# Optimization experiments

Hardware: AMD Instinct MI355X
Metric: run time of the kernel (lower is better)

The kernel has to match this reference:

```python
import jax, jax.numpy as jnp
import numpy as np

EPS = 1e-6
GRID_ORDER_K = 4
DIST_K = 3


def _smallest_k(d, k):
    # k smallest values along last axis, ascending (torch.topk largest=False)
    return -jax.lax.top_k(-d, k)[0]


def _radius_loss(real, fake):
    qs = jnp.array([0.05, 0.1, 0.25, 0.5, 0.75, 0.9, 0.95], jnp.float32)
    fq = jnp.quantile(fake[:, :, 2], qs)
    rq = jnp.quantile(real[:, :, 2], qs)
    return jnp.mean((fq - rq) ** 2)


def _grid_density_loss(real, fake):
    qs = jnp.array([0.05, 0.25, 0.5, 0.75, 0.95], jnp.float32)
    lx = jnp.mean((jnp.quantile(fake[:, :, 0], qs) - jnp.quantile(real[:, :, 0], qs)) ** 2)
    ly = jnp.mean((jnp.quantile(fake[:, :, 1], qs) - jnp.quantile(real[:, :, 1], qs)) ** 2)
    return (lx + ly) / 2


def _knn_dists_flat(x, k):
    # x: [B,N,3]; pairwise dist on xy with +eps under sqrt as in source
    xy = x[:, :, :2]
    d = jnp.sqrt(((xy[:, :, None, :] - xy[:, None, :, :]) ** 2).sum(-1) + EPS)  # [B,N,N]
    d = _smallest_k(d, k)  # [B,N,k]
    return d.reshape(x.shape[0], -1)


def _distance_loss(real, fake):
    qs = jnp.array([0.05, 0.5, 0.95], jnp.float32)
    rq = jnp.quantile(_knn_dists_flat(real, DIST_K), qs, axis=1)  # [3,B]
    fq = jnp.quantile(_knn_dists_flat(fake, DIST_K), qs, axis=1)
    return jnp.mean((fq - rq) ** 2)


def _hexatic_order(coords, k):
    # coords: [B,N,2] -> psi: [B,N] complex
    B, N, _ = coords.shape
    diffs = coords[:, :, None, :] - coords[:, None, :, :]  # [B,N,N,2]
    dx = diffs[..., 0]
    dx = dx + EPS * (jnp.abs(dx) < EPS).astype(dx.dtype)
    angles = jnp.arctan2(diffs[..., 1], dx)
    e_iktheta = jnp.exp(1j * k * angles)  # [B,N,N] complex64
    dist = jnp.sqrt((diffs ** 2).sum(-1) + EPS)
    eye = jnp.eye(N, dtype=bool)[None]
    dist = jnp.where(eye, jnp.inf, dist)
    kth = jax.lax.stop_gradient(_smallest_k(dist, k)[..., -1])  # [B,N]
    sigma = jnp.maximum(0.1 * jnp.maximum(kth[..., None], EPS), EPS)
    arg = jnp.clip((kth[..., None] - dist) / sigma, -50.0, 50.0)
    w = jax.nn.sigmoid(arg)
    psi = (e_iktheta * w).sum(2) / jnp.maximum(w.sum(2), EPS)
    return psi


def _grid_order_loss(samples):
    psi = _hexatic_order(samples[:, :, :2], GRID_ORDER_K)
    return -jnp.mean(jnp.sqrt(psi * jnp.conj(psi))).real


def _physical_feasibility_loss(fake):
    xy = fake[:, :, :2]
    r = fake[:, :, 2]
    N = fake.shape[1]
    sq = ((xy[:, :, None, :] - xy[:, None, :, :]) ** 2).sum(-1)
    d = jnp.sqrt(jnp.where(sq <= 0, 1.0, sq))  # safe sqrt (guard grads at 0)
    d = jnp.where(sq <= 0, 0.0, d)
    tril = jnp.tril(jnp.ones((N, N), bool))[None]
    d = jnp.where(tril, d, 0.0)
    d = jnp.where(d <= 0, jnp.inf, d)
    radii_pair = jnp.abs(r)[:, None, :] + jnp.abs(r)[:, :, None]
    overlap = jax.nn.relu(radii_pair - (d + 1e-4))  # sqrt(x**2)==x for x>=0
    return overlap.sum() / (radii_pair.sum() / 2)


def _gan_loss(fake_outputs):
    t = 0.9  # ones_like - 0.1 label smoothing
    logp = jnp.maximum(jnp.log(fake_outputs), -100.0)
    log1mp = jnp.maximum(jnp.log(1.0 - fake_outputs), -100.0)
    return -jnp.mean(t * logp + (1.0 - t) * log1mp)


def setup_inputs() -> dict:
    key = jax.random.key(0)
    k1, k2, k3 = jax.random.split(key, 3)
    B, N = 4, 2048
    real_images = jax.random.normal(k1, (B, N, 3), jnp.float32)
    fake_images = jax.random.normal(k2, (B, N, 3), jnp.float32)
    fake_outputs = jax.random.uniform(k3, (B, 1), jnp.float32, 1e-3, 1.0 - 1e-3)
    return {"real_images": real_images, "fake_images": fake_images, "fake_outputs": fake_outputs}


def reference(real_images, fake_images, fake_outputs):
    loss = _radius_loss(real_images, fake_images)
    loss = loss + _physical_feasibility_loss(fake_images)
    loss = loss + _gan_loss(fake_outputs)
    loss = loss + _grid_density_loss(real_images, fake_images)
    loss = loss + _distance_loss(real_images, fake_images)
    loss = loss + _grid_order_loss(fake_images)
    return loss
```

## Files before the change

### kernel.cpp

```cpp
#include <hip/hip_runtime.h>
#include <math.h>

#define B_SZ   4
#define N_PTS  2048
#define EPSF   1e-6f

#define WS_KNN_R 0
#define WS_KNN_F 24576
#define WS_FEAS  49152
#define WS_PSIP  50176
#define WS_RSUM  51200
#define WS_Q     51204
#define QZF (WS_Q + 0)
#define QZR (WS_Q + 7)
#define QXF (WS_Q + 14)
#define QXR (WS_Q + 19)
#define QYF (WS_Q + 24)
#define QYR (WS_Q + 29)
#define QDR (WS_Q + 34)
#define QDF (WS_Q + 46)

__constant__ float c_qs7[7] = {0.05f, 0.1f, 0.25f, 0.5f, 0.75f, 0.9f, 0.95f};
__constant__ float c_qs5[5] = {0.05f, 0.25f, 0.5f, 0.75f, 0.95f};
__constant__ float c_qs3[3] = {0.05f, 0.5f, 0.95f};

#define CE(a, b) { float _lo = fminf(a, b), _hi = fmaxf(a, b); a = _lo; b = _hi; }

__device__ __forceinline__ void ins3a(float m[3], float v) {
    float h0 = fmaxf(m[0], v); m[0] = fminf(m[0], v);
    float h1 = fmaxf(m[1], h0); m[1] = fminf(m[1], h0);
    m[2] = fminf(m[2], h1);
}
__device__ __forceinline__ void ins5a(float m[5], float v) {
    float h0 = fmaxf(m[0], v); m[0] = fminf(m[0], v);
    float h1 = fmaxf(m[1], h0); m[1] = fminf(m[1], h0);
    float h2 = fmaxf(m[2], h1); m[2] = fminf(m[2], h1);
    float h3 = fmaxf(m[3], h2); m[3] = fminf(m[3], h2);
    m[4] = fminf(m[4], h3);
}

__device__ __forceinline__ unsigned int tokey(float f) {
    unsigned int u = __float_as_uint(f);
    return (u & 0x80000000u) ? ~u : (u | 0x80000000u);
}
__device__ __forceinline__ float fromkey(unsigned int k) {
    unsigned int u = (k & 0x80000000u) ? (k ^ 0x80000000u) : ~k;
    return __uint_as_float(u);
}

__global__ __launch_bounds__(256) void hs_pair_kernel(const float* __restrict__ real,
                                                      const float* __restrict__ fake,
                                                      float* __restrict__ ws) {
    __shared__ float2 sxy[N_PTS];
    __shared__ float sr[N_PTS];
    __shared__ float red[256];
    const int tid = threadIdx.x, wave = tid >> 6, lane = tid & 63;
    const int blk = blockIdx.x;

    if (blk < 1024) {
        const int b = blk >> 8, grp = blk & 255;
        const float* src = fake + (size_t)b * N_PTS * 3;
        for (int t = tid; t < N_PTS; t += 256) {
            const float* p = src + t * 3;
            sxy[t] = make_float2(p[0], p[1]);
            sr[t]  = fabsf(p[2]);
        }
        __syncthreads();
        const int p0 = grp * 8 + wave * 2;
        float px[2], py[2], pri[2], m[2][5];
#pragma unroll
        for (int t = 0; t < 2; ++t) {
            px[t] = sxy[p0 + t].x; py[t] = sxy[p0 + t].y;
            pri[t] = sr[p0 + t] - 1e-4f;
            m[t][0] = m[t][1] = m[t][2] = m[t][3] = m[t][4] = INFINITY;
        }
        float acc = 0.f;
        for (int j = lane; j < N_PTS; j += 64) {
            float2 q = sxy[j]; float br = sr[j];
#pragma unroll
            for (int t = 0; t < 2; ++t) {
                float dx = px[t] - q.x, dy = py[t] - q.y;
                float sq = fmaf(dx, dx, dy * dy);
                ins5a(m[t], sq);
                float ov = fmaxf((pri[t] + br) - sqrtf(sq), 0.f);
                acc += (sq > 0.f) ? ov : 0.f;
            }
        }
#pragma unroll
        for (int off = 1; off < 64; off <<= 1) {
#pragma unroll
            for (int t = 0; t < 2; ++t) {
                float b0 = __shfl_xor(m[t][0], off);
                float b1 = __shfl_xor(m[t][1], off);
                float b2 = __shfl_xor(m[t][2], off);
                float b3 = __shfl_xor(m[t][3], off);
                float b4 = __shfl_xor(m[t][4], off);
                float l0 = fminf(m[t][0], b4);
                float l1 = fminf(m[t][1], b3);
                float l2 = fminf(m[t][2], b2);
                float l3 = fminf(m[t][3], b1);
                float l4 = fminf(m[t][4], b0);
                CE(l0, l3); CE(l1, l4); CE(l0, l2); CE(l1, l3);
                CE(l0, l1); CE(l2, l4); CE(l1, l2); CE(l3, l4); CE(l2, l3);
                m[t][0] = l0; m[t][1] = l1; m[t][2] = l2; m[t][3] = l3; m[t][4] = l4;
            }
        }
        if (lane == 0) {
            float* kout = ws + WS_KNN_F + b * (N_PTS * 3);
#pragma unroll
            for (int t = 0; t < 2; ++t) {
                const int i = p0 + t;
                kout[i * 3 + 0] = sqrtf(m[t][0] + EPSF);
                kout[i * 3 + 1] = sqrtf(m[t][1] + EPSF);
                kout[i * 3 + 2] = sqrtf(m[t][2] + EPSF);
            }
        }
        float kth[2], invs[2];
#pragma unroll
        for (int t = 0; t < 2; ++t) {
            kth[t] = sqrtf(m[t][4] + EPSF);
            invs[t] = 1.f / fmaxf(0.1f * fmaxf(kth[t], EPSF), EPSF);
        }
        float sw[2], sre[2], sim[2];
#pragma unroll
        for (int t = 0; t < 2; ++t) { sw[t] = 0.f; sre[t] = 0.f; sim[t] = 0.f; }
        for (int j = lane; j < N_PTS; j += 64) {
            float2 q = sxy[j];
#pragma unroll
            for (int t = 0; t < 2; ++t) {
                float dx = px[t] - q.x, dy = py[t] - q.y;
                float sq = fmaf(dx, dx, dy * dy);
                float dist = sqrtf(sq + EPSF);
                dist = (j == p0 + t) ? INFINITY : dist;
                float a = dx + ((fabsf(dx) < EPSF) ? EPSF : 0.f);
                float arg = fminf(fmaxf((kth[t] - dist) * invs[t], -50.f), 50.f);
                float e = __expf(-arg);
                float w = __builtin_amdgcn_rcpf(1.f + e);
                float aa = a * a, bb = dy * dy;
                float n2 = aa + bb;
                float z2r = aa - bb;
                float t0 = a * dy; float z2i = t0 + t0;
                float inv = __builtin_amdgcn_rcpf(n2);
                float ur = z2r * inv, ui = z2i * inv;
                float e4r = fmaf(ur, ur, -(ui * ui));
                float t1 = ur * ui; float e4i = t1 + t1;
                sw[t] += w;
                sre[t] = fmaf(w, e4r, sre[t]);
                sim[t] = fmaf(w, e4i, sim[t]);
            }
        }
#pragma unroll
        for (int off = 1; off < 64; off <<= 1) {
#pragma unroll
            for (int t = 0; t < 2; ++t) {
                sw[t]  += __shfl_xor(sw[t], off);
                sre[t] += __shfl_xor(sre[t], off);
                sim[t] += __shfl_xor(sim[t], off);
            }
        }
        float mypsi = 0.f;
        if (lane == 0) {
#pragma unroll
            for (int t = 0; t < 2; ++t) {
                float den = fmaxf(sw[t], EPSF);
                float pr = sre[t] / den, pi = sim[t] / den;
                mypsi += sqrtf(fmaf(pr, pr, pi * pi));
            }
        }
        red[tid] = acc;
        __syncthreads();
        for (int s = 128; s > 0; s >>= 1) {
            if (tid < s) red[tid] += red[tid + s];
            __syncthreads();
        }
        if (tid == 0) ws[WS_FEAS + blk] = red[0];
        __syncthreads();
        red[tid] = (lane == 0) ? mypsi : 0.f;
        __syncthreads();
        for (int s = 128; s > 0; s >>= 1) {
            if (tid < s) red[tid] += red[tid + s];
            __syncthreads();
        }
        if (tid == 0) ws[WS_PSIP + blk] = red[0];
        if (grp == 0) {
            __syncthreads();
            float rs = 0.f;
            for (int t = tid; t < N_PTS; t += 256) rs += sr[t];
            red[tid] = rs;
            __syncthreads();
            for (int s = 128; s > 0; s >>= 1) {
                if (tid < s) red[tid] += red[tid + s];
                __syncthreads();
            }
            if (tid == 0) ws[WS_RSUM + b] = red[0];
        }
    } else {
        const int rb = blk - 1024;
        const int b = rb >> 7, grp = rb & 127;
        const float* src = real + (size_t)b * N_PTS * 3;
        for (int t = tid; t < N_PTS; t += 256) {
            const float* p = src + t * 3;
            sxy[t] = make_float2(p[0], p[1]);
        }
        __syncthreads();
        const int p0 = grp * 16 + wave * 4;
        float px[4], py[4], m[4][3];
#pragma unroll
        for (int t = 0; t < 4; ++t) {
            px[t] = sxy[p0 + t].x; py[t] = sxy[p0 + t].y;
            m[t][0] = m[t][1] = m[t][2] = INFINITY;
        }
        for (int j = lane; j < N_PTS; j += 64) {
            float2 q = sxy[j];
#pragma unroll
            for (int t = 0; t < 4; ++t) {
                float dx = px[t] - q.x, dy = py[t] - q.y;
                float sq = fmaf(dx, dx, dy * dy);
                ins3a(m[t], sq);
            }
        }
#pragma unroll
        for (int off = 1; off < 64; off <<= 1) {
#pragma unroll
            for (int t = 0; t < 4; ++t) {
                float b0 = __shfl_xor(m[t][0], off);
                float b1 = __shfl_xor(m[t][1], off);
                float b2 = __shfl_xor(m[t][2], off);
                float l0 = fminf(m[t][0], b2);
                float l1 = fminf(m[t][1], b1);
                float l2 = fminf(m[t][2], b0);
                CE(l0, l1); CE(l0, l2); CE(l1, l2);
                m[t][0] = l0; m[t][1] = l1; m[t][2] = l2;
            }
        }
        if (lane == 0) {
            float* kout = ws + WS_KNN_R + b * (N_PTS * 3);
#pragma unroll
            for (int t = 0; t < 4; ++t) {
                const int i = p0 + t;
                kout[i * 3 + 0] = sqrtf(m[t][0] + EPSF);
                kout[i * 3 + 1] = sqrtf(m[t][1] + EPSF);
                kout[i * 3 + 2] = sqrtf(m[t][2] + EPSF);
            }
        }
    }
}

__global__ __launch_bounds__(256) void hs_select_kernel(const float* __restrict__ real,
                                                        const float* __restrict__ fake,
                                                        float* __restrict__ ws) {
    __shared__ unsigned int hist[2048];
    __shared__ unsigned int wtot[4];
    __shared__ unsigned int s_bin, s_rank;
    __shared__ unsigned int s_part[4], s_min[4];
    const int tid = threadIdx.x, wave = tid >> 6, lane = tid & 63;
    const int jb = blockIdx.x;

    const float* src; int step, n, slot; float q;
    if (jb < 34) {
        int aid, qi;
        if (jb < 7)       { aid = 0; qi = jb; }
        else if (jb < 14) { aid = 1; qi = jb - 7; }
        else              { aid = 2 + (jb - 14) / 5; qi = (jb - 14) % 5; }
        const float* base = (aid & 1) ? real : fake;
        const int c = (aid < 2) ? 2 : ((aid < 4) ? 0 : 1);
        src = base + c; step = 3; n = 8192;
        q = (aid < 2) ? c_qs7[qi] : c_qs5[qi];
        slot = ((aid == 0) ? QZF : (aid == 1) ? QZR : (aid == 2) ? QXF
              : (aid == 3) ? QXR : (aid == 4) ? QYF : QYR) + qi;
    } else {
        const int a = jb - 34;
        const int side = a / 12;
        const int b = (a % 12) / 3, qi = a % 3;
        src = ws + (side ? WS_KNN_F : WS_KNN_R) + b * (N_PTS * 3);
        step = 1; n = N_PTS * 3;
        q = c_qs3[qi];
        slot = (side ? QDF : QDR) + b * 3 + qi;
    }

    unsigned int r[32];
#pragma unroll
    for (int u = 0; u < 32; ++u) {
        int e = u * 256 + tid;
        r[u] = (e < n) ? tokey(src[(size_t)e * step]) : 0xFFFFFFFFu;
    }

    const float pos = q * (float)(n - 1);
    const int k = (int)pos;
    const float frac = pos - (float)k;

    unsigned int prefix = 0;
    unsigned int kk = (unsigned int)k;
#pragma unroll
    for (int pass = 0; pass < 3; ++pass) {
        const int shift = (pass == 0) ? 21 : (pass == 1) ? 10 : 0;
        for (int i = tid; i < 2048; i += 256) hist[i] = 0u;
        __syncthreads();
#pragma unroll
        for (int u = 0; u < 32; ++u) {
            unsigned int key = r[u];
            bool act = (pass == 0) ? true
                     : (pass == 1) ? ((key >> 21) == (prefix >> 21))
                                   : ((key >> 10) == (prefix >> 10));
            if (act) atomicAdd(&hist[(key >> shift) & 2047u], 1u);
        }
        __syncthreads();
        unsigned int c[8], psum = 0;
        const int base = tid * 8;
#pragma unroll
        for (int i = 0; i < 8; ++i) { c[i] = hist[base + i]; psum += c[i]; }
        unsigned int v = psum;
#pragma unroll
        for (int off = 1; off < 64; off <<= 1) {
            unsigned int nb = (unsigned int)__shfl_up((int)v, off);
            if (lane >= off) v += nb;
        }
        if (lane == 63) wtot[wave] = v;
        __syncthreads();
        unsigned int woff = 0;
        for (int w2 = 0; w2 < wave; ++w2) woff += wtot[w2];
        unsigned int incl = v + woff;
        unsigned int excl = incl - psum;
        if (excl <= kk && kk < incl) {
            unsigned int cum = excl;
#pragma unroll
            for (int i = 0; i < 8; ++i) {
                if (kk < cum + c[i]) { s_bin = (unsigned int)(base + i); s_rank = kk - cum; break; }
                cum += c[i];
            }
        }
        __syncthreads();
        prefix |= s_bin << shift;
        kk = s_rank;
        __syncthreads();
    }
    const unsigned int vk = prefix;

    unsigned int cle = 0, mg = 0xFFFFFFFFu;
#pragma unroll
    for (int u = 0; u < 32; ++u) {
        cle += (r[u] <= vk) ? 1u : 0u;
        if (r[u] > vk && r[u] < mg) mg = r[u];
    }
#pragma unroll
    for (int off = 1; off < 64; off <<= 1) {
        cle += (unsigned int)__shfl_xor((int)cle, off);
        unsigned int om = (unsigned int)__shfl_xor((int)mg, off);
        mg = (om < mg) ? om : mg;
    }
    if (lane == 0) { s_part[wave] = cle; s_min[wave] = mg; }
    __syncthreads();
    if (tid == 0) {
        unsigned int tot = s_part[0] + s_part[1] + s_part[2] + s_part[3];
        unsigned int mga = s_min[0];
        if (s_min[1] < mga) mga = s_min[1];
        if (s_min[2] < mga) mga = s_min[2];
        if (s_min[3] < mga) mga = s_min[3];
        unsigned int vhi = (tot >= (unsigned int)(k + 2)) ? vk : mga;
        float flo = fromkey(vk), fhi = fromkey(vhi);
        ws[slot] = flo + frac * (fhi - flo);
    }
}

__global__ __launch_bounds__(256) void hs_final_kernel(const float* __restrict__ fouts,
                                                       const float* __restrict__ ws,
                                                       float* __restrict__ out) {
    __shared__ float red[256];
    __shared__ float s_feas;
    const int tid = threadIdx.x;
    float fs = 0.f, ps = 0.f;
    for (int t = tid; t < 1024; t += 256) {
        fs += ws[WS_FEAS + t];
        ps += ws[WS_PSIP + t];
    }
    red[tid] = fs;
    __syncthreads();
    for (int s = 128; s > 0; s >>= 1) {
        if (tid < s) red[tid] += red[tid + s];
        __syncthreads();
    }
    if (tid == 0) s_feas = red[0];
    __syncthreads();
    red[tid] = ps;
    __syncthreads();
    for (int s = 128; s > 0; s >>= 1) {
        if (tid < s) red[tid] += red[tid + s];
        __syncthreads();
    }
    if (tid == 0) {
        float psi_sum = red[0];
        float rsum = ws[WS_RSUM + 0] + ws[WS_RSUM + 1] + ws[WS_RSUM + 2] + ws[WS_RSUM + 3];
        float loss = 0.f;
        float sacc = 0.f;
        for (int q = 0; q < 7; ++q) { float d = ws[QZF + q] - ws[QZR + q]; sacc += d * d; }
        loss += sacc / 7.f;
        loss += (0.5f * s_feas) / ((float)N_PTS * rsum);
        float g = 0.f;
        for (int b = 0; b < B_SZ; ++b) {
            float p = fouts[b];
            g += 0.9f * fmaxf(logf(p), -100.f) + 0.1f * fmaxf(logf(1.f - p), -100.f);
        }
        loss += -g / (float)B_SZ;
        float sx = 0.f, sy = 0.f;
        for (int q = 0; q < 5; ++q) {
            float dx = ws[QXF + q] - ws[QXR + q]; sx += dx * dx;
            float dy = ws[QYF + q] - ws[QYR + q]; sy += dy * dy;
        }
        loss += 0.5f * (sx / 5.f + sy / 5.f);
        float sd = 0.f;
        for (int t = 0; t < 12; ++t) { float d = ws[QDF + t] - ws[QDR + t]; sd += d * d; }
        loss += sd / 12.f;
        loss += -psi_sum / (float)(B_SZ * N_PTS);
        out[0] = loss;
    }
}

extern "C" void kernel_launch(void* const* d_in, const int* in_sizes, int n_in,
                              void* d_out, int out_size, void* d_ws, size_t ws_size,
                              hipStream_t stream) {
    (void)in_sizes; (void)n_in; (void)out_size; (void)ws_size;
    const float* real  = (const float*)d_in[0];
    const float* fake  = (const float*)d_in[1];
    const float* fouts = (const float*)d_in[2];
    float* out = (float*)d_out;
    float* ws  = (float*)d_ws;

    hipLaunchKernelGGL(hs_pair_kernel,   dim3(1536), dim3(256), 0, stream, real, fake, ws);
    hipLaunchKernelGGL(hs_select_kernel, dim3(58),   dim3(256), 0, stream, real, fake, ws);
    hipLaunchKernelGGL(hs_final_kernel,  dim3(1),    dim3(256), 0, stream, fouts, ws, out);
}
```

Measured before the change: 121.6 us.

## Rewrite quantile select as single-wave 8-bit radix select with LDS keys

Reworks the quantile selection kernel to use one 64-lane wave per block, storing keys in shared memory and running a four-pass 8-bit radix select with replicated histograms. Cross-wave synchronisation and shared scalar handoffs are replaced by wave-level ballot and shuffle. This removes block-level barriers and reduces atomic contention, but each block now processes all keys with a quarter of the threads and one extra pass.

```diff
diff --git a/kernel.cpp b/kernel.cpp
--- a/kernel.cpp
+++ b/kernel.cpp
@@ -246,14 +246,12 @@
     }
 }
 
-__global__ __launch_bounds__(256) void hs_select_kernel(const float* __restrict__ real,
-                                                        const float* __restrict__ fake,
-                                                        float* __restrict__ ws) {
+__global__ __launch_bounds__(64) void hs_select_kernel(const float* __restrict__ real,
+                                                       const float* __restrict__ fake,
+                                                       float* __restrict__ ws) {
+    __shared__ unsigned int skey[8192];
     __shared__ unsigned int hist[2048];
-    __shared__ unsigned int wtot[4];
-    __shared__ unsigned int s_bin, s_rank;
-    __shared__ unsigned int s_part[4], s_min[4];
-    const int tid = threadIdx.x, wave = tid >> 6, lane = tid & 63;
+    const int lane = threadIdx.x;
     const int jb = blockIdx.x;
 
     const float* src; int step, n, slot; float q;
@@ -278,69 +276,84 @@
         slot = (side ? QDF : QDR) + b * 3 + qi;
     }
 
-    unsigned int r[32];
-#pragma unroll
-    for (int u = 0; u < 32; ++u) {
-        int e = u * 256 + tid;
-        r[u] = (e < n) ? tokey(src[(size_t)e * step]) : 0xFFFFFFFFu;
-    }
+#pragma unroll 4
+    for (int it = 0; it < 128; ++it) {
+        const int e = it * 64 + lane;
+        skey[e] = (e < n) ? tokey(src[(size_t)e * step]) : 0xFFFFFFFFu;
+    }
+    __syncthreads();
 
     const float pos = q * (float)(n - 1);
     const int k = (int)pos;
     const float frac = pos - (float)k;
 
-    unsigned int prefix = 0;
+    unsigned int prefix = 0u;
     unsigned int kk = (unsigned int)k;
-#pragma unroll
-    for (int pass = 0; pass < 3; ++pass) {
-        const int shift = (pass == 0) ? 21 : (pass == 1) ? 10 : 0;
-        for (int i = tid; i < 2048; i += 256) hist[i] = 0u;
-        __syncthreads();
-#pragma unroll
-        for (int u = 0; u < 32; ++u) {
-            unsigned int key = r[u];
-            bool act = (pass == 0) ? true
-                     : (pass == 1) ? ((key >> 21) == (prefix >> 21))
-                                   : ((key >> 10) == (prefix >> 10));
-            if (act) atomicAdd(&hist[(key >> shift) & 2047u], 1u);
-        }
-        __syncthreads();
-        unsigned int c[8], psum = 0;
-        const int base = tid * 8;
-#pragma unroll
-        for (int i = 0; i < 8; ++i) { c[i] = hist[base + i]; psum += c[i]; }
-        unsigned int v = psum;
+    const unsigned int rep = (unsigned int)(lane & 7);
+#pragma unroll
+    for (int pass = 0; pass < 4; ++pass) {
+        const int shift = 24 - 8 * pass;
+        const unsigned int amask = (pass == 0) ? 0u : (pass == 1) ? 0xFF000000u
+                                 : (pass == 2) ? 0xFFFF0000u : 0xFFFFFF00u;
+#pragma unroll
+        for (int i = 0; i < 32; ++i) hist[i * 64 + lane] = 0u;
+        __syncthreads();
+        for (int it = 0; it < 128; ++it) {
+            const unsigned int key = skey[it * 64 + lane];
+            if (((key ^ prefix) & amask) == 0u) {
+                const unsigned int bin = (key >> shift) & 255u;
+                atomicAdd(&hist[bin * 8u + rep], 1u);
+            }
+        }
+        __syncthreads();
+        unsigned int c[4], psum = 0;
+#pragma unroll
+        for (int i = 0; i < 4; ++i) {
+            const uint4* hp = (const uint4*)&hist[(lane * 4 + i) * 8];
+            uint4 a = hp[0], b2 = hp[1];
+            c[i] = a.x + a.y + a.z + a.w + b2.x + b2.y + b2.z + b2.w;
+            psum += c[i];
+        }
+        unsigned int incl = psum;
 #pragma unroll
         for (int off = 1; off < 64; off <<= 1) {
-            unsigned int nb = (unsigned int)__shfl_up((int)v, off);
-            if (lane >= off) v += nb;
-        }
-        if (lane == 63) wtot[wave] = v;
-        __syncthreads();
-        unsigned int woff = 0;
-        for (int w2 = 0; w2 < wave; ++w2) woff += wtot[w2];
-        unsigned int incl = v + woff;
-        unsigned int excl = incl - psum;
-        if (excl <= kk && kk < incl) {
+            unsigned int nb = (unsigned int)__shfl_up((int)incl, off);
+            if (lane >= off) incl += nb;
+        }
+        const unsigned int excl = incl - psum;
+        const bool has = (excl <= kk) && (kk < incl);
+        unsigned long long bmask = __ballot(has);
+        const int srcl = (int)__ffsll((long long)bmask) - 1;
+        unsigned int bsel = 0, rsel = 0;
+        if (has) {
             unsigned int cum = excl;
 #pragma unroll
-            for (int i = 0; i < 8; ++i) {
-                if (kk < cum + c[i]) { s_bin = (unsigned int)(base + i); s_rank = kk - cum; break; }
+            for (int i = 0; i < 4; ++i) {
+                if (kk >= cum && kk < cum + c[i]) { bsel = (unsigned int)(lane * 4 + i); rsel = kk - cum; }
                 cum += c[i];
             }
         }
-        __syncthreads();
-        prefix |= s_bin << shift;
-        kk = s_rank;
+        bsel = (unsigned int)__shfl((int)bsel, srcl);
+        rsel = (unsigned int)__shfl((int)rsel, srcl);
+        prefix |= bsel << shift;
+        kk = rsel;
         __syncthreads();
     }
     const unsigned int vk = prefix;
 
     unsigned int cle = 0, mg = 0xFFFFFFFFu;
-#pragma unroll
-    for (int u = 0; u < 32; ++u) {
-        cle += (r[u] <= vk) ? 1u : 0u;
-        if (r[u] > vk && r[u] < mg) mg = r[u];
+    const uint4* kp = (const uint4*)skey;
+#pragma unroll 4
+    for (int it = 0; it < 32; ++it) {
+        uint4 v = kp[it * 64 + lane];
+        cle += (v.x <= vk) ? 1u : 0u;
+        cle += (v.y <= vk) ? 1u : 0u;
+        cle += (v.z <= vk) ? 1u : 0u;
+        cle += (v.w <= vk) ? 1u : 0u;
+        if (v.x > vk && v.x < mg) mg = v.x;
+        if (v.y > vk && v.y < mg) mg = v.y;
+        if (v.z > vk && v.z < mg) mg = v.z;
+        if (v.w > vk && v.w < mg) mg = v.w;
     }
 #pragma unroll
     for (int off = 1; off < 64; off <<= 1) {
@@ -348,16 +361,9 @@
         unsigned int om = (unsigned int)__shfl_xor((int)mg, off);
         mg = (om < mg) ? om : mg;
     }
-    if (lane == 0) { s_part[wave] = cle; s_min[wave] = mg; }
-    __syncthreads();
-    if (tid == 0) {
-        unsigned int tot = s_part[0] + s_part[1] + s_part[2] + s_part[3];
-        unsigned int mga = s_min[0];
-        if (s_min[1] < mga) mga = s_min[1];
-        if (s_min[2] < mga) mga = s_min[2];
-        if (s_min[3] < mga) mga = s_min[3];
-        unsigned int vhi = (tot >= (unsigned int)(k + 2)) ? vk : mga;
-        float flo = fromkey(vk), fhi = fromkey(vhi);
+    if (lane == 0) {
+        const unsigned int vhi = (cle >= (unsigned int)(k + 2)) ? vk : mg;
+        const float flo = fromkey(vk), fhi = fromkey(vhi);
         ws[slot] = flo + frac * (fhi - flo);
     }
 }
@@ -426,6 +432,6 @@
     float* ws  = (float*)d_ws;
 
     hipLaunchKernelGGL(hs_pair_kernel,   dim3(1536), dim3(256), 0, stream, real, fake, ws);
-    hipLaunchKernelGGL(hs_select_kernel, dim3(58),   dim3(256), 0, stream, real, fake, ws);
+    hipLaunchKernelGGL(hs_select_kernel, dim3(58),   dim3(64),  0, stream, real, fake, ws);
     hipLaunchKernelGGL(hs_final_kernel,  dim3(1),    dim3(256), 0, stream, fouts, ws, out);
 }
```

Result: slower. 165.9 us (+36.4%).

## Fuse final reduction into select kernel and use 8-bit radix passes with replicated histograms

Applied to the files above, without the earlier changes.

The separate final kernel is removed. Its reduction now runs in the last-arriving block of the select kernel, chosen through a global atomic counter that the pair kernel resets. The select kernel moves to 1024 threads with four 8-bit radix passes over per-wave, lane-parity-replicated histograms, which cuts shared-memory atomic contention and register use per thread. The aim is to save a kernel launch and shorten the serial quantile selection, at the cost of threadfence handshaking and an extra radix pass.

```diff
diff --git a/kernel.cpp b/kernel.cpp
--- a/kernel.cpp
+++ b/kernel.cpp
@@ -11,6 +11,7 @@
 #define WS_PSIP  50176
 #define WS_RSUM  51200
 #define WS_Q     51204
+#define WS_CNT   51264
 #define QZF (WS_Q + 0)
 #define QZR (WS_Q + 7)
 #define QXF (WS_Q + 14)
@@ -56,6 +57,7 @@
     __shared__ float red[256];
     const int tid = threadIdx.x, wave = tid >> 6, lane = tid & 63;
     const int blk = blockIdx.x;
+    if (blk == 0 && tid == 0) ((unsigned int*)ws)[WS_CNT] = 0u;
 
     if (blk < 1024) {
         const int b = blk >> 8, grp = blk & 255;
@@ -246,13 +248,16 @@
     }
 }
 
-__global__ __launch_bounds__(256) void hs_select_kernel(const float* __restrict__ real,
-                                                        const float* __restrict__ fake,
-                                                        float* __restrict__ ws) {
-    __shared__ unsigned int hist[2048];
-    __shared__ unsigned int wtot[4];
+__global__ __launch_bounds__(1024) void hs_select_kernel(const float* __restrict__ real,
+                                                         const float* __restrict__ fake,
+                                                         const float* __restrict__ fouts,
+                                                         float* __restrict__ ws,
+                                                         float* __restrict__ out) {
+    __shared__ unsigned int hist[16][256][2];
     __shared__ unsigned int s_bin, s_rank;
-    __shared__ unsigned int s_part[4], s_min[4];
+    __shared__ unsigned int s_part[16], s_min[16];
+    __shared__ float sred[1024];
+    __shared__ int s_last;
     const int tid = threadIdx.x, wave = tid >> 6, lane = tid & 63;
     const int jb = blockIdx.x;
 
@@ -278,69 +283,76 @@
         slot = (side ? QDF : QDR) + b * 3 + qi;
     }
 
-    unsigned int r[32];
-#pragma unroll
-    for (int u = 0; u < 32; ++u) {
-        int e = u * 256 + tid;
-        r[u] = (e < n) ? tokey(src[(size_t)e * step]) : 0xFFFFFFFFu;
+    unsigned int rr[8];
+#pragma unroll
+    for (int u = 0; u < 8; ++u) {
+        const int e = u * 1024 + tid;
+        rr[u] = (e < n) ? tokey(src[(size_t)e * step]) : 0xFFFFFFFFu;
     }
 
     const float pos = q * (float)(n - 1);
     const int k = (int)pos;
     const float frac = pos - (float)k;
 
-    unsigned int prefix = 0;
+    unsigned int prefix = 0u;
     unsigned int kk = (unsigned int)k;
-#pragma unroll
-    for (int pass = 0; pass < 3; ++pass) {
-        const int shift = (pass == 0) ? 21 : (pass == 1) ? 10 : 0;
-        for (int i = tid; i < 2048; i += 256) hist[i] = 0u;
-        __syncthreads();
-#pragma unroll
-        for (int u = 0; u < 32; ++u) {
-            unsigned int key = r[u];
-            bool act = (pass == 0) ? true
-                     : (pass == 1) ? ((key >> 21) == (prefix >> 21))
-                                   : ((key >> 10) == (prefix >> 10));
-            if (act) atomicAdd(&hist[(key >> shift) & 2047u], 1u);
-        }
-        __syncthreads();
-        unsigned int c[8], psum = 0;
-        const int base = tid * 8;
-#pragma unroll
-        for (int i = 0; i < 8; ++i) { c[i] = hist[base + i]; psum += c[i]; }
-        unsigned int v = psum;
-#pragma unroll
-        for (int off = 1; off < 64; off <<= 1) {
-            unsigned int nb = (unsigned int)__shfl_up((int)v, off);
-            if (lane >= off) v += nb;
-        }
-        if (lane == 63) wtot[wave] = v;
-        __syncthreads();
-        unsigned int woff = 0;
-        for (int w2 = 0; w2 < wave; ++w2) woff += wtot[w2];
-        unsigned int incl = v + woff;
-        unsigned int excl = incl - psum;
-        if (excl <= kk && kk < incl) {
-            unsigned int cum = excl;
-#pragma unroll
-            for (int i = 0; i < 8; ++i) {
-                if (kk < cum + c[i]) { s_bin = (unsigned int)(base + i); s_rank = kk - cum; break; }
-                cum += c[i];
+    const unsigned int rep = (unsigned int)(lane & 1);
+#pragma unroll
+    for (int pass = 0; pass < 4; ++pass) {
+        const int shift = 24 - 8 * pass;
+        const unsigned int amask = (pass == 0) ? 0u : (pass == 1) ? 0xFF000000u
+                                 : (pass == 2) ? 0xFFFF0000u : 0xFFFFFF00u;
+        unsigned int* hflat = &hist[0][0][0];
+#pragma unroll
+        for (int i = 0; i < 8; ++i) hflat[i * 1024 + tid] = 0u;
+        __syncthreads();
+#pragma unroll
+        for (int u = 0; u < 8; ++u) {
+            const unsigned int key = rr[u];
+            if (((key ^ prefix) & amask) == 0u)
+                atomicAdd(&hist[wave][(key >> shift) & 255u][rep], 1u);
+        }
+        __syncthreads();
+        if (tid < 64) {
+            unsigned int c[4], ps = 0;
+#pragma unroll
+            for (int i = 0; i < 4; ++i) {
+                unsigned int s = 0;
+                const int bin = lane * 4 + i;
+#pragma unroll
+                for (int w = 0; w < 16; ++w) {
+                    uint2 v = *(const uint2*)&hist[w][bin][0];
+                    s += v.x + v.y;
+                }
+                c[i] = s; ps += s;
+            }
+            unsigned int incl = ps;
+#pragma unroll
+            for (int off = 1; off < 64; off <<= 1) {
+                unsigned int nb = (unsigned int)__shfl_up((int)incl, off);
+                if (lane >= off) incl += nb;
+            }
+            const unsigned int excl = incl - ps;
+            if (excl <= kk && kk < incl) {
+                unsigned int cum = excl;
+#pragma unroll
+                for (int i = 0; i < 4; ++i) {
+                    if (kk < cum + c[i]) { s_bin = (unsigned int)(lane * 4 + i); s_rank = kk - cum; break; }
+                    cum += c[i];
+                }
             }
         }
         __syncthreads();
         prefix |= s_bin << shift;
         kk = s_rank;
-        __syncthreads();
     }
     const unsigned int vk = prefix;
 
     unsigned int cle = 0, mg = 0xFFFFFFFFu;
 #pragma unroll
-    for (int u = 0; u < 32; ++u) {
-        cle += (r[u] <= vk) ? 1u : 0u;
-        if (r[u] > vk && r[u] < mg) mg = r[u];
+    for (int u = 0; u < 8; ++u) {
+        cle += (rr[u] <= vk) ? 1u : 0u;
+        if (rr[u] > vk && rr[u] < mg) mg = rr[u];
     }
 #pragma unroll
     for (int off = 1; off < 64; off <<= 1) {
@@ -351,48 +363,48 @@
     if (lane == 0) { s_part[wave] = cle; s_min[wave] = mg; }
     __syncthreads();
     if (tid == 0) {
-        unsigned int tot = s_part[0] + s_part[1] + s_part[2] + s_part[3];
-        unsigned int mga = s_min[0];
-        if (s_min[1] < mga) mga = s_min[1];
-        if (s_min[2] < mga) mga = s_min[2];
-        if (s_min[3] < mga) mga = s_min[3];
-        unsigned int vhi = (tot >= (unsigned int)(k + 2)) ? vk : mga;
-        float flo = fromkey(vk), fhi = fromkey(vhi);
+        unsigned int tot = 0, mga = 0xFFFFFFFFu;
+#pragma unroll
+        for (int w = 0; w < 16; ++w) {
+            tot += s_part[w];
+            if (s_min[w] < mga) mga = s_min[w];
+        }
+        const unsigned int vhi = (tot >= (unsigned int)(k + 2)) ? vk : mga;
+        const float flo = fromkey(vk), fhi = fromkey(vhi);
         ws[slot] = flo + frac * (fhi - flo);
     }
-}
-
-__global__ __launch_bounds__(256) void hs_final_kernel(const float* __restrict__ fouts,
-                                                       const float* __restrict__ ws,
-                                                       float* __restrict__ out) {
-    __shared__ float red[256];
-    __shared__ float s_feas;
-    const int tid = threadIdx.x;
-    float fs = 0.f, ps = 0.f;
-    for (int t = tid; t < 1024; t += 256) {
-        fs += ws[WS_FEAS + t];
-        ps += ws[WS_PSIP + t];
-    }
-    red[tid] = fs;
+
+    __threadfence();
+    if (tid == 0) {
+        unsigned int t = atomicAdd(&((unsigned int*)ws)[WS_CNT], 1u);
+        s_last = (t == 57u) ? 1 : 0;
+    }
     __syncthreads();
-    for (int s = 128; s > 0; s >>= 1) {
-        if (tid < s) red[tid] += red[tid + s];
-        __syncthreads();
-    }
-    if (tid == 0) s_feas = red[0];
+    if (!s_last) return;
+    __threadfence();
+
+    float fs = ws[WS_FEAS + tid];
+    float ps = ws[WS_PSIP + tid];
+    sred[tid] = fs;
     __syncthreads();
-    red[tid] = ps;
+    for (int s = 512; s > 0; s >>= 1) {
+        if (tid < s) sred[tid] += sred[tid + s];
+        __syncthreads();
+    }
+    float s_feas = sred[0];
     __syncthreads();
-    for (int s = 128; s > 0; s >>= 1) {
-        if (tid < s) red[tid] += red[tid + s];
+    sred[tid] = ps;
+    __syncthreads();
+    for (int s = 512; s > 0; s >>= 1) {
+        if (tid < s) sred[tid] += sred[tid + s];
         __syncthreads();
     }
     if (tid == 0) {
-        float psi_sum = red[0];
+        float psi_sum = sred[0];
         float rsum = ws[WS_RSUM + 0] + ws[WS_RSUM + 1] + ws[WS_RSUM + 2] + ws[WS_RSUM + 3];
         float loss = 0.f;
         float sacc = 0.f;
-        for (int q = 0; q < 7; ++q) { float d = ws[QZF + q] - ws[QZR + q]; sacc += d * d; }
+        for (int qq = 0; qq < 7; ++qq) { float d = ws[QZF + qq] - ws[QZR + qq]; sacc += d * d; }
         loss += sacc / 7.f;
         loss += (0.5f * s_feas) / ((float)N_PTS * rsum);
         float g = 0.f;
@@ -402,9 +414,9 @@
         }
         loss += -g / (float)B_SZ;
         float sx = 0.f, sy = 0.f;
-        for (int q = 0; q < 5; ++q) {
-            float dx = ws[QXF + q] - ws[QXR + q]; sx += dx * dx;
-            float dy = ws[QYF + q] - ws[QYR + q]; sy += dy * dy;
+        for (int qq = 0; qq < 5; ++qq) {
+            float dx = ws[QXF + qq] - ws[QXR + qq]; sx += dx * dx;
+            float dy = ws[QYF + qq] - ws[QYR + qq]; sy += dy * dy;
         }
         loss += 0.5f * (sx / 5.f + sy / 5.f);
         float sd = 0.f;
@@ -425,7 +437,6 @@
     float* out = (float*)d_out;
     float* ws  = (float*)d_ws;
 
-    hipLaunchKernelGGL(hs_pair_kernel,   dim3(1536), dim3(256), 0, stream, real, fake, ws);
-    hipLaunchKernelGGL(hs_select_kernel, dim3(58),   dim3(256), 0, stream, real, fake, ws);
-    hipLaunchKernelGGL(hs_final_kernel,  dim3(1),    dim3(256), 0, stream, fouts, ws, out);
-}
+    hipLaunchKernelGGL(hs_pair_kernel,   dim3(1536), dim3(256),  0, stream, real, fake, ws);
+    hipLaunchKernelGGL(hs_select_kernel, dim3(58),   dim3(1024), 0, stream, real, fake, fouts, ws, out);
+}
```

Measured after the change: 133.2 us. 1.1x slower.
